# Kernel optimization log

Measured on AMD Instinct MI355X. Metric: run time of the kernel, lower is better.

## Reference

```python
import jax, jax.numpy as jnp
import numpy as np


def setup_inputs() -> dict:
    key = jax.random.key(0)
    ks = jax.random.split(key, 6)
    B_, S, D_in, D_out, R, E = 4, 2048, 2048, 2048, 64, 16
    x = jax.random.normal(ks[0], (B_, S, D_in), dtype=jnp.float32)
    W_base = jax.random.normal(ks[1], (D_out, D_in), dtype=jnp.float32) * (D_in ** -0.5)
    b_base = jax.random.normal(ks[2], (D_out,), dtype=jnp.float32) * 0.02
    # orthogonal rows, as get_orthogonal_matrix(reservoir_size, in_features)
    G = np.asarray(jax.random.normal(ks[3], (D_in, R), dtype=jnp.float32))
    Q, _ = np.linalg.qr(G)  # [D_in, R] orthonormal columns
    A = jnp.asarray(Q.T, dtype=jnp.float32)  # [R, D_in]
    # B initialized to zeros in the module; use small random so delta is nontrivial
    Bmat = jax.random.normal(ks[4], (E, D_out, R), dtype=jnp.float32) * 0.02
    W_router = jax.random.normal(ks[5], (E, D_in), dtype=jnp.float32) * 0.02
    return {"x": x, "W_base": W_base, "b_base": b_base, "A": A, "B": Bmat,
            "W_router": W_router, "top_k": 2}


def reference(x, W_base, b_base, A, B, W_router, top_k):
    E = W_router.shape[0]
    base_output = jnp.einsum('bsi,oi->bso', x, W_base) + b_base          # [B,S,D_out]
    res_hidden = jnp.einsum('bsi,ri->bsr', x, A)                          # [B,S,R]
    router_logits = jnp.einsum('bsi,ei->bse', x, W_router)                # [B,S,E]
    routing_weights = jax.nn.softmax(router_logits, axis=-1)
    if top_k > 0 and top_k < E:
        _, top_idx = jax.lax.top_k(routing_weights, top_k)                # [B,S,k]
        mask = jax.nn.one_hot(top_idx, E, dtype=routing_weights.dtype).sum(axis=-2)
        routing_weights = routing_weights * mask
        routing_weights = routing_weights / (routing_weights.sum(axis=-1, keepdims=True) + 1e-6)
    # contract experts+rank without materializing [B,S,E,D_out]
    h = jnp.einsum('bsr,bse->bser', res_hidden, routing_weights)          # [B,S,E,R] (small)
    delta = jnp.einsum('bser,edr->bsd', h, B)                             # [B,S,D_out]
    return base_output + delta
```

## Files before the change

kernel.cpp:

```cpp
#include <hip/hip_runtime.h>
#include <hip/hip_bf16.h>

#define D_IN  2048
#define D_OUT 2048
#define RNK   64
#define NE    16
#define KTOT  3072
#define NTILE 48

typedef __attribute__((ext_vector_type(8))) short bf16x8;
typedef __attribute__((ext_vector_type(4))) float f32x4;

__device__ __forceinline__ void async_ld16(const void* g, void* l) {
    __builtin_amdgcn_global_load_lds(
        (const __attribute__((address_space(1))) void*)g,
        (__attribute__((address_space(3))) void*)l,
        16, 0, 0);
}

__global__ __launch_bounds__(384) void castwa_kernel(
    const float* __restrict__ Wb, const float* __restrict__ Bm,
    const float* __restrict__ A,
    __hip_bfloat16* __restrict__ Wc, __hip_bfloat16* __restrict__ Ab)
{
    const int c = threadIdx.x * 8;
    const float* src;
    __hip_bfloat16* dst;
    if (blockIdx.x < D_OUT) {
        const int n = blockIdx.x;
        if (c < D_IN) {
            src = Wb + (size_t)n * D_IN + c;
        } else {
            const int j = c - D_IN;
            const int e = j >> 6, r = j & 63;
            src = Bm + ((size_t)e * D_OUT + n) * RNK + r;
        }
        dst = Wc + (size_t)n * KTOT + c;
    } else {
        if (c >= D_IN) return;
        const int r = blockIdx.x - D_OUT;
        src = A + (size_t)r * D_IN + c;
        dst = Ab + (size_t)r * D_IN + c;
    }
    const float4 a = *(const float4*)src;
    const float4 b = *(const float4*)(src + 4);
    const float vv[8] = {a.x, a.y, a.z, a.w, b.x, b.y, b.z, b.w};
    union { bf16x8 v; __hip_bfloat16 h[8]; } u;
#pragma unroll
    for (int q = 0; q < 8; ++q) u.h[q] = __float2bfloat16(vv[q]);
    *(bf16x8*)dst = u.v;
}

__global__ __launch_bounds__(512) void prep2_kernel(
    const float* __restrict__ x, const float* __restrict__ Wr,
    const __hip_bfloat16* __restrict__ Ab,
    const int* __restrict__ topk_p, __hip_bfloat16* __restrict__ Xc)
{
    __shared__ __align__(16) char smem[81920];
    __hip_bfloat16* xb = (__hip_bfloat16*)smem;
    float* stage = (float*)(smem + 65536);
    float* red = (float*)smem;
    float* wf  = (float*)(smem + 65536);

    const int tid = threadIdx.x;
    const int wave = tid >> 6, lane = tid & 63;
    const int qm = lane & 15, quad = lane >> 4;
    const int t0 = blockIdx.x * 16;
    const int tA = t0 + wave * 2;

    float acc[NE][2];
#pragma unroll
    for (int e = 0; e < NE; ++e) { acc[e][0] = 0.f; acc[e][1] = 0.f; }

    const float4* x4 = (const float4*)x;
    float4 xv[2], xn[2];
    xv[0] = x4[(size_t)tA * 512 + lane];
    xv[1] = x4[(size_t)(tA + 1) * 512 + lane];

    for (int c = 0; c < 8; ++c) {
        async_ld16(Wr + (size_t)wave * D_IN + c * 256 + lane * 4,
                   (void*)(stage + wave * 256));
        async_ld16(Wr + (size_t)(wave + 8) * D_IN + c * 256 + lane * 4,
                   (void*)(stage + (wave + 8) * 256));
        if (c < 7) {
            xn[0] = x4[(size_t)tA * 512 + (c + 1) * 64 + lane];
            xn[1] = x4[(size_t)(tA + 1) * 512 + (c + 1) * 64 + lane];
        }
        __syncthreads();

#pragma unroll
        for (int t = 0; t < 2; ++t) {
            const int tl = wave * 2 + t;
            union { short4 v; __hip_bfloat16 h[4]; } u;
            u.h[0] = __float2bfloat16(xv[t].x); u.h[1] = __float2bfloat16(xv[t].y);
            u.h[2] = __float2bfloat16(xv[t].z); u.h[3] = __float2bfloat16(xv[t].w);
            *(short4*)(Xc + (size_t)(t0 + tl) * KTOT + c * 256 + lane * 4) = u.v;
            const int gg = c * 32 + (lane >> 1);
            const int pg = gg ^ (tl & 7);
            *(short4*)((char*)xb + tl * 4096 + pg * 16 + (lane & 1) * 8) = u.v;
        }
        const float4* wr4 = (const float4*)stage;
#pragma unroll
        for (int e = 0; e < NE; ++e) {
            const float4 wv = wr4[e * 64 + lane];
            acc[e][0] += xv[0].x*wv.x + xv[0].y*wv.y + xv[0].z*wv.z + xv[0].w*wv.w;
            acc[e][1] += xv[1].x*wv.x + xv[1].y*wv.y + xv[1].z*wv.z + xv[1].w*wv.w;
        }
        __syncthreads();
        if (c < 7) { xv[0] = xn[0]; xv[1] = xn[1]; }
    }

#pragma unroll
    for (int off = 32; off; off >>= 1)
#pragma unroll
        for (int e = 0; e < NE; ++e) {
            acc[e][0] += __shfl_xor(acc[e][0], off, 64);
            acc[e][1] += __shfl_xor(acc[e][1], off, 64);
        }
    if (lane < 2) {
        const int tt = lane;
        const int k = topk_p[0];
        float m = -1e30f;
#pragma unroll
        for (int e = 0; e < NE; ++e) m = fmaxf(m, acc[e][tt]);
        float w[NE]; float ssum = 0.f;
#pragma unroll
        for (int e = 0; e < NE; ++e) { w[e] = __expf(acc[e][tt] - m); ssum += w[e]; }
        const float inv = 1.f / ssum;
#pragma unroll
        for (int e = 0; e < NE; ++e) w[e] *= inv;
        float* wfout = wf + (size_t)(wave * 2 + tt) * NE;
        if (k > 0 && k < NE) {
            int chosen[NE];
#pragma unroll
            for (int e = 0; e < NE; ++e) chosen[e] = 0;
            float ksum = 0.f;
            for (int it = 0; it < k; ++it) {
                int bi = 0; float bv = -1.f;
                for (int e = 0; e < NE; ++e)
                    if (!chosen[e] && w[e] > bv) { bv = w[e]; bi = e; }
                chosen[bi] = 1; ksum += bv;
            }
            const float rinv = 1.f / (ksum + 1e-6f);
            for (int e = 0; e < NE; ++e) wfout[e] = chosen[e] ? w[e] * rinv : 0.f;
        } else {
            for (int e = 0; e < NE; ++e) wfout[e] = w[e];
        }
    }

    f32x4 racc[4] = {};
    const int kb = wave * 256;
#pragma unroll
    for (int s = 0; s < 4; ++s) {
        const int k0 = kb + s * 64;
        const int gg0 = (k0 >> 3) + quad;
        const bf16x8 a0 = *(const bf16x8*)((char*)xb + qm * 4096 + ((gg0 ^ (qm & 7)) * 16));
        const bf16x8 a1 = *(const bf16x8*)((char*)xb + qm * 4096 + (((gg0 + 4) ^ (qm & 7)) * 16));
        bf16x8 b0[4], b1[4];
#pragma unroll
        for (int nf = 0; nf < 4; ++nf) {
            const __hip_bfloat16* bp = Ab + (size_t)(qm + nf * 16) * D_IN + k0 + quad * 8;
            b0[nf] = *(const bf16x8*)bp;
            b1[nf] = *(const bf16x8*)(bp + 32);
        }
#pragma unroll
        for (int nf = 0; nf < 4; ++nf) {
            racc[nf] = __builtin_amdgcn_mfma_f32_16x16x32_bf16(a0, b0[nf], racc[nf], 0, 0, 0);
            racc[nf] = __builtin_amdgcn_mfma_f32_16x16x32_bf16(a1, b1[nf], racc[nf], 0, 0, 0);
        }
    }
    __syncthreads();

#pragma unroll
    for (int nf = 0; nf < 4; ++nf)
#pragma unroll
        for (int r = 0; r < 4; ++r)
            red[(wave * 16 + quad * 4 + r) * 64 + nf * 16 + qm] = racc[nf][r];
    __syncthreads();

#pragma unroll
    for (int it = 0; it < 4; ++it) {
        const int s = it * 512 + tid;
        const int t = s >> 7;
        const int chunk = s & 127;
        const int e = chunk >> 3, r0 = (chunk & 7) * 8;
        const float wgt = wf[t * 16 + e];
        float4 s0 = {0.f, 0.f, 0.f, 0.f}, s1 = {0.f, 0.f, 0.f, 0.f};
#pragma unroll
        for (int w2 = 0; w2 < 8; ++w2) {
            const float4 p0 = ((const float4*)red)[(w2 * 16 + t) * 16 + (r0 >> 2)];
            const float4 p1 = ((const float4*)red)[(w2 * 16 + t) * 16 + (r0 >> 2) + 1];
            s0.x += p0.x; s0.y += p0.y; s0.z += p0.z; s0.w += p0.w;
            s1.x += p1.x; s1.y += p1.y; s1.z += p1.z; s1.w += p1.w;
        }
        union { bf16x8 v; __hip_bfloat16 h[8]; } u;
        u.h[0] = __float2bfloat16(wgt * s0.x); u.h[1] = __float2bfloat16(wgt * s0.y);
        u.h[2] = __float2bfloat16(wgt * s0.z); u.h[3] = __float2bfloat16(wgt * s0.w);
        u.h[4] = __float2bfloat16(wgt * s1.x); u.h[5] = __float2bfloat16(wgt * s1.y);
        u.h[6] = __float2bfloat16(wgt * s1.z); u.h[7] = __float2bfloat16(wgt * s1.w);
        *(bf16x8*)(Xc + (size_t)(t0 + t) * KTOT + D_IN + chunk * 8) = u.v;
    }
}

#define LDA(BO, MH, i, kk) (*(const bf16x8*)(ldsc + (BO) + \
    ((MH) * 128 + wm2 * 64 + (i) * 16 + qm) * 128 + \
    ((((kk) * 4 + quad) ^ (qm & 7)) * 16)))
#define LDB(BO, NH, j, kk) (*(const bf16x8*)(ldsc + 65536 + (BO) + \
    ((NH) * 128 + wn4 * 32 + (j) * 16 + qm) * 128 + \
    ((((kk) * 4 + quad) ^ (qm & 7)) * 16)))

#define PHASE(BO, MH, NH, STAGE_STMT, WAIT_STMT) do { \
    bf16x8 af0[4], bv0[2], af1[4], bv1[2]; \
    _Pragma("unroll") for (int i = 0; i < 4; ++i) af0[i] = LDA(BO, MH, i, 0); \
    _Pragma("unroll") for (int j = 0; j < 2; ++j) bv0[j] = LDB(BO, NH, j, 0); \
    STAGE_STMT; \
    WAIT_STMT; \
    __builtin_amdgcn_sched_barrier(0); \
    __builtin_amdgcn_s_barrier(); \
    __builtin_amdgcn_sched_barrier(0); \
    __builtin_amdgcn_s_setprio(1); \
    _Pragma("unroll") for (int i = 0; i < 4; ++i) \
    _Pragma("unroll") for (int j = 0; j < 2; ++j) \
        acc[(MH)*4+i][(NH)*2+j] = __builtin_amdgcn_mfma_f32_16x16x32_bf16( \
            af0[i], bv0[j], acc[(MH)*4+i][(NH)*2+j], 0, 0, 0); \
    _Pragma("unroll") for (int i = 0; i < 4; ++i) af1[i] = LDA(BO, MH, i, 1); \
    _Pragma("unroll") for (int j = 0; j < 2; ++j) bv1[j] = LDB(BO, NH, j, 1); \
    _Pragma("unroll") for (int i = 0; i < 4; ++i) \
    _Pragma("unroll") for (int j = 0; j < 2; ++j) \
        acc[(MH)*4+i][(NH)*2+j] = __builtin_amdgcn_mfma_f32_16x16x32_bf16( \
            af1[i], bv1[j], acc[(MH)*4+i][(NH)*2+j], 0, 0, 0); \
    __builtin_amdgcn_s_setprio(0); \
    __builtin_amdgcn_sched_barrier(0); \
    __builtin_amdgcn_s_barrier(); \
    __builtin_amdgcn_sched_barrier(0); \
} while (0)

__global__ __launch_bounds__(512, 2) void gemm2_kernel(
    const __hip_bfloat16* __restrict__ Am,
    const __hip_bfloat16* __restrict__ Bm,
    const float* __restrict__ bias,
    float* __restrict__ C)
{
    __shared__ __align__(16) char smem[131072];
    char* ldsc = smem;
    const int tid = threadIdx.x;
    const int w = tid >> 6, lane = tid & 63;
    const int qm = lane & 15, quad = lane >> 4;
    const int wm2 = w >> 2, wn4 = w & 3;

    int flat = blockIdx.y * gridDim.x + blockIdx.x;
    flat = (flat & 7) * 32 + (flat >> 3);
    const int bm = flat & 31, bn = flat >> 5;

    const int rb0 = w * 16 + (lane >> 3);
    const int rb1 = rb0 + 8;
    const int gs0 = (lane & 7) ^ (rb0 & 7);
    const int gs1 = (lane & 7) ^ (rb1 & 7);
    const __hip_bfloat16* pA0 = Am + (size_t)(bm * 256 + rb0) * KTOT + gs0 * 8;
    const __hip_bfloat16* pA1 = Am + (size_t)(bm * 256 + rb1) * KTOT + gs1 * 8;
    const __hip_bfloat16* pB0 = Bm + (size_t)(bn * 256 + rb0) * KTOT + gs0 * 8;
    const __hip_bfloat16* pB1 = Bm + (size_t)(bn * 256 + rb1) * KTOT + gs1 * 8;

    f32x4 acc[8][4] = {};

    auto stage_pair = [&](int tn, int hh) {
        const size_t ko = (size_t)tn * 64;
        const size_t ho = (size_t)hh * (128 * KTOT);
        char* da = ldsc + (tn & 1) * 32768 + hh * 16384 + w * 2048;
        async_ld16(pA0 + ho + ko, da);
        async_ld16(pA1 + ho + ko, da + 1024);
        char* db = ldsc + 65536 + (tn & 1) * 32768 + hh * 16384 + w * 2048;
        async_ld16(pB0 + ho + ko, db);
        async_ld16(pB1 + ho + ko, db + 1024);
    };

    stage_pair(0, 0); stage_pair(0, 1);
    asm volatile("s_waitcnt vmcnt(0)" ::: "memory");
    __builtin_amdgcn_s_barrier();

    for (int t = 0; t < NTILE - 1; ++t) {
        const int bo = (t & 1) * 32768;
        PHASE(bo, 0, 0, stage_pair(t + 1, 0),
              asm volatile("s_waitcnt vmcnt(4)" ::: "memory"));
        PHASE(bo, 1, 0, stage_pair(t + 1, 1), );
        PHASE(bo, 0, 1, , );
        PHASE(bo, 1, 1, ,
              asm volatile("s_waitcnt vmcnt(4)" ::: "memory"));
    }
    {
        const int bo = 32768;
        PHASE(bo, 0, 0, , asm volatile("s_waitcnt vmcnt(0)" ::: "memory"));
        PHASE(bo, 1, 0, , );
        PHASE(bo, 0, 1, , );
        PHASE(bo, 1, 1, , );
    }

    const size_t row0 = (size_t)bm * 256;
    const int col0 = bn * 256;
#pragma unroll
    for (int nh = 0; nh < 2; ++nh)
#pragma unroll
    for (int j = 0; j < 2; ++j) {
        const int col = col0 + nh * 128 + wn4 * 32 + j * 16 + qm;
        const float bb = bias[col];
#pragma unroll
        for (int mh = 0; mh < 2; ++mh)
#pragma unroll
        for (int i = 0; i < 4; ++i) {
#pragma unroll
            for (int r = 0; r < 4; ++r) {
                const size_t row = row0 + mh * 128 + wm2 * 64 + i * 16 + quad * 4 + r;
                C[row * D_OUT + col] = acc[mh * 4 + i][nh * 2 + j][r] + bb;
            }
        }
    }
}

extern "C" void kernel_launch(void* const* d_in, const int* in_sizes, int n_in,
                              void* d_out, int out_size, void* d_ws, size_t ws_size,
                              hipStream_t stream) {
    const float* x    = (const float*)d_in[0];
    const float* Wb   = (const float*)d_in[1];
    const float* bb   = (const float*)d_in[2];
    const float* A    = (const float*)d_in[3];
    const float* Bm   = (const float*)d_in[4];
    const float* Wr   = (const float*)d_in[5];
    const int*   topk = (const int*)d_in[6];
    float* out = (float*)d_out;
    const int T = in_sizes[0] / D_IN;

    __hip_bfloat16* Xc = (__hip_bfloat16*)d_ws;
    __hip_bfloat16* Wc = (__hip_bfloat16*)((char*)d_ws + (size_t)T * KTOT * 2);
    __hip_bfloat16* Ab = (__hip_bfloat16*)d_out;

    castwa_kernel<<<D_OUT + RNK, 384, 0, stream>>>(Wb, Bm, A, Wc, Ab);
    prep2_kernel<<<T / 16, 512, 0, stream>>>(x, Wr, Ab, topk, Xc);
    gemm2_kernel<<<dim3(32, 8), 512, 0, stream>>>(Xc, Wc, bb, out);
}
```

Before: 277.7 us.

## Switch GEMM to 32x32x16 MFMA with two-phase staged pipeline

Rewrites the main GEMM inner loop to use 32x32x16 bf16 MFMA instructions with 16-wide accumulators instead of 16x16x32, loading B fragments once per K-tile and reusing them across both M halves. The LDS staging is restructured into two uneven stages (A half plus all of B, then the other A half), issued with a deeper prefetch distance and fewer barriers per tile. This aims to cut LDS read traffic and barrier overhead per MFMA. It raises register pressure from holding persistent B fragments and complicates the vmcnt accounting.

```diff
diff --git a/kernel.cpp b/kernel.cpp
--- a/kernel.cpp
+++ b/kernel.cpp
@@ -10,6 +10,7 @@
 
 typedef __attribute__((ext_vector_type(8))) short bf16x8;
 typedef __attribute__((ext_vector_type(4))) float f32x4;
+typedef __attribute__((ext_vector_type(16))) float f32x16;
 
 __device__ __forceinline__ void async_ld16(const void* g, void* l) {
     __builtin_amdgcn_global_load_lds(
@@ -202,50 +203,47 @@
     }
 }
 
-#define LDA(BO, MH, i, kk) (*(const bf16x8*)(ldsc + (BO) + \
-    ((MH) * 128 + wm2 * 64 + (i) * 16 + qm) * 128 + \
-    ((((kk) * 4 + quad) ^ (qm & 7)) * 16)))
-#define LDB(BO, NH, j, kk) (*(const bf16x8*)(ldsc + 65536 + (BO) + \
-    ((NH) * 128 + wn4 * 32 + (j) * 16 + qm) * 128 + \
-    ((((kk) * 4 + quad) ^ (qm & 7)) * 16)))
-
-#define PHASE(BO, MH, NH, STAGE_STMT, WAIT_STMT) do { \
-    bf16x8 af0[4], bv0[2], af1[4], bv1[2]; \
-    _Pragma("unroll") for (int i = 0; i < 4; ++i) af0[i] = LDA(BO, MH, i, 0); \
-    _Pragma("unroll") for (int j = 0; j < 2; ++j) bv0[j] = LDB(BO, NH, j, 0); \
-    STAGE_STMT; \
-    WAIT_STMT; \
-    __builtin_amdgcn_sched_barrier(0); \
-    __builtin_amdgcn_s_barrier(); \
-    __builtin_amdgcn_sched_barrier(0); \
+#define LDA3(BUF, M, ks) (*(const bf16x8*)(smem + (BUF) + \
+    ((((M) >> 1) * 128 + wm2 * 64 + ((M) & 1) * 32 + l31) * 128) + \
+    (((((ks) * 2 + lhi) ^ (l31 & 7))) << 4)))
+#define LDB3(BUF, N, ks) (*(const bf16x8*)(smem + 65536 + (BUF) + \
+    ((wn4 * 64 + (N) * 32 + l31) * 128) + \
+    (((((ks) * 2 + lhi) ^ (l31 & 7))) << 4)))
+
+#define GP(BUF, MH, ISSUE, WAIT) do { \
+    bf16x8 af[2][4]; \
+    if ((MH) == 0) { \
+        _Pragma("unroll") for (int n = 0; n < 2; ++n) \
+        _Pragma("unroll") for (int ks = 0; ks < 4; ++ks) \
+            bfr[n][ks] = LDB3(BUF, n, ks); \
+    } \
+    _Pragma("unroll") for (int m = 0; m < 2; ++m) \
+    _Pragma("unroll") for (int ks = 0; ks < 4; ++ks) \
+        af[m][ks] = LDA3(BUF, (MH) * 2 + m, ks); \
+    ISSUE; \
     __builtin_amdgcn_s_setprio(1); \
-    _Pragma("unroll") for (int i = 0; i < 4; ++i) \
-    _Pragma("unroll") for (int j = 0; j < 2; ++j) \
-        acc[(MH)*4+i][(NH)*2+j] = __builtin_amdgcn_mfma_f32_16x16x32_bf16( \
-            af0[i], bv0[j], acc[(MH)*4+i][(NH)*2+j], 0, 0, 0); \
-    _Pragma("unroll") for (int i = 0; i < 4; ++i) af1[i] = LDA(BO, MH, i, 1); \
-    _Pragma("unroll") for (int j = 0; j < 2; ++j) bv1[j] = LDB(BO, NH, j, 1); \
-    _Pragma("unroll") for (int i = 0; i < 4; ++i) \
-    _Pragma("unroll") for (int j = 0; j < 2; ++j) \
-        acc[(MH)*4+i][(NH)*2+j] = __builtin_amdgcn_mfma_f32_16x16x32_bf16( \
-            af1[i], bv1[j], acc[(MH)*4+i][(NH)*2+j], 0, 0, 0); \
+    _Pragma("unroll") for (int ks = 0; ks < 4; ++ks) \
+    _Pragma("unroll") for (int m = 0; m < 2; ++m) \
+    _Pragma("unroll") for (int n = 0; n < 2; ++n) \
+        acc[(MH) * 2 + m][n] = __builtin_amdgcn_mfma_f32_32x32x16_bf16( \
+            af[m][ks], bfr[n][ks], acc[(MH) * 2 + m][n], 0, 0, 0); \
     __builtin_amdgcn_s_setprio(0); \
+    WAIT; \
     __builtin_amdgcn_sched_barrier(0); \
     __builtin_amdgcn_s_barrier(); \
     __builtin_amdgcn_sched_barrier(0); \
 } while (0)
 
-__global__ __launch_bounds__(512, 2) void gemm2_kernel(
+__global__ __launch_bounds__(512, 2) void gemm3_kernel(
     const __hip_bfloat16* __restrict__ Am,
     const __hip_bfloat16* __restrict__ Bm,
     const float* __restrict__ bias,
     float* __restrict__ C)
 {
     __shared__ __align__(16) char smem[131072];
-    char* ldsc = smem;
     const int tid = threadIdx.x;
     const int w = tid >> 6, lane = tid & 63;
-    const int qm = lane & 15, quad = lane >> 4;
+    const int l31 = lane & 31, lhi = lane >> 5;
     const int wm2 = w >> 2, wn4 = w & 3;
 
     int flat = blockIdx.y * gridDim.x + blockIdx.x;
@@ -260,57 +258,68 @@
     const __hip_bfloat16* pA1 = Am + (size_t)(bm * 256 + rb1) * KTOT + gs1 * 8;
     const __hip_bfloat16* pB0 = Bm + (size_t)(bn * 256 + rb0) * KTOT + gs0 * 8;
     const __hip_bfloat16* pB1 = Bm + (size_t)(bn * 256 + rb1) * KTOT + gs1 * 8;
-
-    f32x4 acc[8][4] = {};
-
-    auto stage_pair = [&](int tn, int hh) {
+    const size_t HO = (size_t)128 * KTOT;
+
+    f32x16 acc[4][2] = {};
+    bf16x8 bfr[2][4];
+
+    auto stageP1 = [&](int tn) {
         const size_t ko = (size_t)tn * 64;
-        const size_t ho = (size_t)hh * (128 * KTOT);
-        char* da = ldsc + (tn & 1) * 32768 + hh * 16384 + w * 2048;
-        async_ld16(pA0 + ho + ko, da);
-        async_ld16(pA1 + ho + ko, da + 1024);
-        char* db = ldsc + 65536 + (tn & 1) * 32768 + hh * 16384 + w * 2048;
-        async_ld16(pB0 + ho + ko, db);
-        async_ld16(pB1 + ho + ko, db + 1024);
+        char* da = smem + (tn & 1) * 32768 + w * 2048;
+        async_ld16(pA0 + ko, da);
+        async_ld16(pA1 + ko, da + 1024);
+        char* db = smem + 65536 + (tn & 1) * 32768 + w * 2048;
+        async_ld16(pB0 + ko, db);
+        async_ld16(pB1 + ko, db + 1024);
+        async_ld16(pB0 + HO + ko, db + 16384);
+        async_ld16(pB1 + HO + ko, db + 16384 + 1024);
     };
-
-    stage_pair(0, 0); stage_pair(0, 1);
-    asm volatile("s_waitcnt vmcnt(0)" ::: "memory");
+    auto stageP2 = [&](int tn) {
+        const size_t ko = (size_t)tn * 64;
+        char* da = smem + (tn & 1) * 32768 + 16384 + w * 2048;
+        async_ld16(pA0 + HO + ko, da);
+        async_ld16(pA1 + HO + ko, da + 1024);
+    };
+
+    stageP1(0); stageP2(0); stageP1(1);
+    asm volatile("s_waitcnt vmcnt(8)" ::: "memory");
+    __builtin_amdgcn_sched_barrier(0);
     __builtin_amdgcn_s_barrier();
-
-    for (int t = 0; t < NTILE - 1; ++t) {
+    __builtin_amdgcn_sched_barrier(0);
+
+    for (int t = 0; t < NTILE - 2; ++t) {
         const int bo = (t & 1) * 32768;
-        PHASE(bo, 0, 0, stage_pair(t + 1, 0),
-              asm volatile("s_waitcnt vmcnt(4)" ::: "memory"));
-        PHASE(bo, 1, 0, stage_pair(t + 1, 1), );
-        PHASE(bo, 0, 1, , );
-        PHASE(bo, 1, 1, ,
-              asm volatile("s_waitcnt vmcnt(4)" ::: "memory"));
+        GP(bo, 0, stageP2(t + 1),
+           asm volatile("s_waitcnt vmcnt(8)" ::: "memory"));
+        GP(bo, 1, stageP1(t + 2),
+           asm volatile("s_waitcnt vmcnt(8)" ::: "memory"));
     }
     {
-        const int bo = 32768;
-        PHASE(bo, 0, 0, , asm volatile("s_waitcnt vmcnt(0)" ::: "memory"));
-        PHASE(bo, 1, 0, , );
-        PHASE(bo, 0, 1, , );
-        PHASE(bo, 1, 1, , );
-    }
-
-    const size_t row0 = (size_t)bm * 256;
-    const int col0 = bn * 256;
-#pragma unroll
-    for (int nh = 0; nh < 2; ++nh)
-#pragma unroll
-    for (int j = 0; j < 2; ++j) {
-        const int col = col0 + nh * 128 + wn4 * 32 + j * 16 + qm;
-        const float bb = bias[col];
-#pragma unroll
-        for (int mh = 0; mh < 2; ++mh)
-#pragma unroll
-        for (int i = 0; i < 4; ++i) {
-#pragma unroll
-            for (int r = 0; r < 4; ++r) {
-                const size_t row = row0 + mh * 128 + wm2 * 64 + i * 16 + quad * 4 + r;
-                C[row * D_OUT + col] = acc[mh * 4 + i][nh * 2 + j][r] + bb;
+        const int bo = ((NTILE - 2) & 1) * 32768;
+        GP(bo, 0, stageP2(NTILE - 1),
+           asm volatile("s_waitcnt vmcnt(8)" ::: "memory"));
+        GP(bo, 1, ,
+           asm volatile("s_waitcnt vmcnt(2)" ::: "memory"));
+    }
+    {
+        const int bo = ((NTILE - 1) & 1) * 32768;
+        GP(bo, 0, ,
+           asm volatile("s_waitcnt vmcnt(0)" ::: "memory"));
+        GP(bo, 1, , );
+    }
+
+#pragma unroll
+    for (int n = 0; n < 2; ++n) {
+        const int col = bn * 256 + wn4 * 64 + n * 32 + l31;
+        const float bbv = bias[col];
+#pragma unroll
+        for (int m = 0; m < 4; ++m) {
+            const size_t rbase = (size_t)bm * 256 + (m >> 1) * 128 + wm2 * 64
+                               + (m & 1) * 32 + 4 * lhi;
+#pragma unroll
+            for (int reg = 0; reg < 16; ++reg) {
+                const size_t row = rbase + (reg & 3) + 8 * (reg >> 2);
+                C[row * D_OUT + col] = acc[m][n][reg] + bbv;
             }
         }
     }
@@ -335,5 +344,5 @@
 
     castwa_kernel<<<D_OUT + RNK, 384, 0, stream>>>(Wb, Bm, A, Wc, Ab);
     prep2_kernel<<<T / 16, 512, 0, stream>>>(x, Wr, Ab, topk, Xc);
-    gemm2_kernel<<<dim3(32, 8), 512, 0, stream>>>(Xc, Wc, bb, out);
-}
+    gemm3_kernel<<<dim3(32, 8), 512, 0, stream>>>(Xc, Wc, bb, out);
+}
```

Result: faster. 265.5 us (-4.4%).
